# Performance work log

Hardware: AMD Instinct MI355X
Metric: run time of the kernel (lower is better)

Reference implementation:

```python
import jax, jax.numpy as jnp
import numpy as np

# Module configuration (from init_kwargs)
NLAT_IN, NLON_IN = 181, 360
NLAT_OUT, NLON_OUT = 361, 720
KSIZE = 3            # kernel_size of piecewise-linear basis with kernel_shape=3
CIN, COUT = 16, 16   # groups=1 -> groupsize = CIN
NNZ = 8192           # nonzeros in the precomputed psi tensor
B = 1


def setup_inputs() -> dict:
    key = jax.random.key(0)
    ks = jax.random.split(key, 6)
    x = jax.random.normal(ks[0], (B, CIN, NLAT_IN, NLON_IN), dtype=jnp.float32)
    # weight init: sqrt(1/groupsize) * basis init factors * randn
    scale = np.float32(np.sqrt(1.0 / CIN))
    weight = scale * jax.random.normal(ks[1], (COUT, CIN, KSIZE), dtype=jnp.float32)
    bias = jnp.zeros((COUT,), dtype=jnp.float32)
    # synthetic COO psi tensor (geometry-free but structurally identical)
    ker_idx = jax.random.randint(ks[2], (NNZ,), 0, KSIZE, dtype=jnp.int32)
    row_idx = jax.random.randint(ks[3], (NNZ,), 0, NLAT_IN, dtype=jnp.int32)
    col_idx = jax.random.randint(ks[4], (NNZ,), 0, NLAT_OUT * NLON_OUT, dtype=jnp.int32)
    vals = jax.random.uniform(ks[5], (NNZ,), dtype=jnp.float32) * (100.0 / NNZ)
    return {"x": x, "weight": weight, "bias": bias,
            "ker_idx": ker_idx, "row_idx": row_idx, "col_idx": col_idx, "vals": vals}


def reference(x, weight, bias, ker_idx, row_idx, col_idx, vals):
    """DISCO transpose conv on S2: channel-mix einsum, then sparse
    gather-multiply-scatter (adjoint of the longitude-shift-equivariant
    sparse contraction). col_idx encodes (out_lat, lon_offset)."""
    Bb, Cin, H, W = x.shape            # (B, C_in, nlat_in, nlon_in)
    Cout, gs, K = weight.shape
    pscale = NLON_OUT // W             # exact p-shift upsampling factor

    # 1) channel mixing with per-kernel-basis weights (groups=1)
    xw = jnp.einsum('bcxy,ock->bokxy', x, weight)   # [B, Cout, K, nlat_in, nlon_in]

    # 2) gather rows referenced by the sparse psi tensor and scale by vals
    g = xw[:, :, ker_idx, row_idx, :] * vals[None, None, :, None]  # [B, Cout, NNZ, W]

    # 3) scatter-add: each nonzero (k, tin, (tout, p)) contributes the whole
    #    longitude ring of input lat tin to output lat tout at lons (p + po*pscale)
    hi = col_idx // NLON_OUT                      # output latitude  [NNZ]
    p = col_idx % NLON_OUT                        # longitude offset [NNZ]
    lon = (p[:, None] + jnp.arange(W, dtype=p.dtype)[None, :] * pscale) % NLON_OUT  # [NNZ, W]
    flat = (hi[:, None] * NLON_OUT + lon).reshape(-1)  # [NNZ*W]

    out = jnp.zeros((Bb, Cout, NLAT_OUT * NLON_OUT), dtype=x.dtype)
    out = out.at[:, :, flat].add(g.reshape(Bb, Cout, -1))
    out = out.reshape(Bb, Cout, NLAT_OUT, NLON_OUT)
    return out + bias[None, :, None, None]
```

## Files before the change

kernel.cpp:

```cpp
#include <hip/hip_runtime.h>

#define H_IN   181
#define W_IN   360
#define NLAT   361
#define NLON   720
#define CIN    16
#define COUT   16
#define KSZ    3
#define NNZ    8192
#define MAXB   64
#define SLICE_E (KSZ * H_IN * W_IN * 4)
#define NMIX_BLK ((KSZ * H_IN * W_IN + 255) / 256)

static __device__ __forceinline__ unsigned short f2bf(float f) {
    unsigned int u = __float_as_uint(f);
    u = (u + 0x7fffu + ((u >> 16) & 1u)) >> 16;
    return (unsigned short)u;
}
static __device__ __forceinline__ void bf2_to_f2(unsigned int d, float& lo, float& hi) {
    lo = __uint_as_float(d << 16);
    hi = __uint_as_float(d & 0xffff0000u);
}

__global__ __launch_bounds__(256) void mix_bucket_kernel(
    const float* __restrict__ x,
    const float* __restrict__ w,
    const int*   __restrict__ ker_idx,
    const int*   __restrict__ row_idx,
    const int*   __restrict__ col_idx,
    const float* __restrict__ vals,
    unsigned short* __restrict__ xw,
    int*   __restrict__ gcnt,
    int*   __restrict__ gbase,
    int*   __restrict__ gp,
    float* __restrict__ gv)
{
    const int tid = threadIdx.x;

    if (blockIdx.x >= NMIX_BLK) {
        const int ho = blockIdx.x - NMIX_BLK;
        __shared__ int s_cnt;
        if (tid == 0) s_cnt = 0;
        __syncthreads();
        const int4* col4 = (const int4*)col_idx;
        for (int n4 = tid; n4 < NNZ / 4; n4 += 256) {
            const int4 c4 = col4[n4];
#pragma unroll
            for (int j = 0; j < 4; ++j) {
                const int c  = (j == 0) ? c4.x : (j == 1) ? c4.y : (j == 2) ? c4.z : c4.w;
                const int hi = c / NLON;
                if (hi == ho) {
                    const int n    = 4 * n4 + j;
                    const int slot = atomicAdd(&s_cnt, 1);
                    if (slot < MAXB) {
                        gbase[ho * MAXB + slot] = (ker_idx[n] * H_IN + row_idx[n]) * (W_IN * 4);
                        gp[ho * MAXB + slot]    = c - hi * NLON;
                        gv[ho * MAXB + slot]    = vals[n];
                    }
                }
            }
        }
        __syncthreads();
        if (tid == 0) gcnt[ho] = (s_cnt < MAXB) ? s_cnt : MAXB;
        return;
    }

    __shared__ float sw[COUT * CIN * KSZ];
    for (int i = tid; i < COUT * CIN * KSZ; i += 256) sw[i] = w[i];
    __syncthreads();

    const int idx = blockIdx.x * 256 + tid;
    if (idx >= KSZ * H_IN * W_IN) return;
    const int k  = idx / (H_IN * W_IN);
    const int hy = idx - k * (H_IN * W_IN);

    float acc[COUT];
#pragma unroll
    for (int co = 0; co < COUT; ++co) acc[co] = 0.f;

    for (int c = 0; c < CIN; ++c) {
        const float xv = x[c * (H_IN * W_IN) + hy];
#pragma unroll
        for (int co = 0; co < COUT; ++co)
            acc[co] += xv * sw[(co * CIN + c) * KSZ + k];
    }

#pragma unroll
    for (int q = 0; q < 4; ++q) {
        ushort4 b;
        b.x = f2bf(acc[4*q+0]); b.y = f2bf(acc[4*q+1]);
        b.z = f2bf(acc[4*q+2]); b.w = f2bf(acc[4*q+3]);
        *(ushort4*)(xw + (size_t)q * SLICE_E + (size_t)idx * 4) = b;
    }
}

__device__ __forceinline__ void fma4(float4& a, float v, const float4& f) {
    a.x += v * f.x; a.y += v * f.y; a.z += v * f.z; a.w += v * f.w;
}
static __device__ __forceinline__ float4 ld_bf4(const unsigned short* p) {
    const uint2 d = *(const uint2*)p;
    float4 f;
    bf2_to_f2(d.x, f.x, f.y);
    bf2_to_f2(d.y, f.z, f.w);
    return f;
}

__global__ __launch_bounds__(384) void gather_kernel(
    const unsigned short* __restrict__ xw,
    const float* __restrict__ bias,
    const int*   __restrict__ gcnt,
    const int*   __restrict__ gbase,
    const int*   __restrict__ gp,
    const float* __restrict__ gv,
    float* __restrict__ out)
{
    const int ho  = blockIdx.x >> 2;
    const int q   = blockIdx.x & 3;
    const int tid = threadIdx.x;

    __shared__ int   s_base[MAXB];
    __shared__ int   s_p[MAXB];
    __shared__ float s_v[MAXB];

    const int cnt = gcnt[ho];
    if (tid < cnt) {
        s_base[tid] = gbase[ho * MAXB + tid];
        s_p[tid]    = gp[ho * MAXB + tid];
        s_v[tid]    = gv[ho * MAXB + tid];
    }
    __syncthreads();

    if (tid >= 360) return;
    const int lo0 = 2 * tid;

    const float4 bq = ((const float4*)bias)[q];
    float4 accE = bq, accO = bq;
    const unsigned short* slice = xw + (size_t)q * SLICE_E;

    auto entry_y = [&](int p, int b) -> int {
        int d = (lo0 + b) - p;
        if (d < 0) d += NLON;
        return d >> 1;
    };

    int e = 0;
    for (; e + 2 <= cnt; e += 2) {
        const int   p0 = s_p[e],   p1 = s_p[e + 1];
        const float v0 = s_v[e],   v1 = s_v[e + 1];
        const int   b0 = p0 & 1,   b1 = p1 & 1;
        const int   y0 = entry_y(p0, b0);
        const int   y1 = entry_y(p1, b1);
        const float4 f0 = ld_bf4(slice + s_base[e]     + y0 * 4);
        const float4 f1 = ld_bf4(slice + s_base[e + 1] + y1 * 4);
        if (b0 == 0) fma4(accE, v0, f0); else fma4(accO, v0, f0);
        if (b1 == 0) fma4(accE, v1, f1); else fma4(accO, v1, f1);
    }
    if (e < cnt) {
        const int   p = s_p[e];
        const float v = s_v[e];
        const int   b = p & 1;
        const int   y = entry_y(p, b);
        const float4 f = ld_bf4(slice + s_base[e] + y * 4);
        if (b == 0) fma4(accE, v, f); else fma4(accO, v, f);
    }

    const float2 r[4] = { make_float2(accE.x, accO.x), make_float2(accE.y, accO.y),
                          make_float2(accE.z, accO.z), make_float2(accE.w, accO.w) };
#pragma unroll
    for (int j = 0; j < 4; ++j) {
        const int co = 4 * q + j;
        *(float2*)(out + ((size_t)co * NLAT + ho) * NLON + lo0) = r[j];
    }
}

extern "C" void kernel_launch(void* const* d_in, const int* in_sizes, int n_in,
                              void* d_out, int out_size, void* d_ws, size_t ws_size,
                              hipStream_t stream) {
    const float* x       = (const float*)d_in[0];
    const float* weight  = (const float*)d_in[1];
    const float* bias    = (const float*)d_in[2];
    const int*   ker_idx = (const int*)d_in[3];
    const int*   row_idx = (const int*)d_in[4];
    const int*   col_idx = (const int*)d_in[5];
    const float* vals    = (const float*)d_in[6];
    float* out = (float*)d_out;

    unsigned short* xw = (unsigned short*)d_ws;
    int*   gcnt  = (int*)((char*)d_ws + 6255360 + 64);
    int*   gbase = gcnt + 512;
    int*   gp    = gbase + NLAT * MAXB;
    float* gv    = (float*)(gp + NLAT * MAXB);

    mix_bucket_kernel<<<NMIX_BLK + NLAT, 256, 0, stream>>>(
        x, weight, ker_idx, row_idx, col_idx, vals, xw, gcnt, gbase, gp, gv);
    gather_kernel<<<NLAT * 4, 384, 0, stream>>>(xw, bias, gcnt, gbase, gp, gv, out);
}
```

Measured before the change: 99.23 us.

## Fuse mixing and gather into one kernel, applying channel mix after sparse gather

```diff
diff --git a/kernel.cpp b/kernel.cpp
--- a/kernel.cpp
+++ b/kernel.cpp
@@ -9,167 +9,93 @@
 #define KSZ    3
 #define NNZ    8192
 #define MAXB   64
-#define SLICE_E (KSZ * H_IN * W_IN * 4)
-#define NMIX_BLK ((KSZ * H_IN * W_IN + 255) / 256)
+#define XPLANE (H_IN * W_IN)
 
-static __device__ __forceinline__ unsigned short f2bf(float f) {
-    unsigned int u = __float_as_uint(f);
-    u = (u + 0x7fffu + ((u >> 16) & 1u)) >> 16;
-    return (unsigned short)u;
-}
-static __device__ __forceinline__ void bf2_to_f2(unsigned int d, float& lo, float& hi) {
-    lo = __uint_as_float(d << 16);
-    hi = __uint_as_float(d & 0xffff0000u);
-}
-
-__global__ __launch_bounds__(256) void mix_bucket_kernel(
+__global__ __launch_bounds__(384) void fused_disco_kernel(
     const float* __restrict__ x,
     const float* __restrict__ w,
+    const float* __restrict__ bias,
     const int*   __restrict__ ker_idx,
     const int*   __restrict__ row_idx,
     const int*   __restrict__ col_idx,
     const float* __restrict__ vals,
-    unsigned short* __restrict__ xw,
-    int*   __restrict__ gcnt,
-    int*   __restrict__ gbase,
-    int*   __restrict__ gp,
-    float* __restrict__ gv)
+    float* __restrict__ out)
 {
+    const int ho  = blockIdx.x >> 1;
+    const int pe  = blockIdx.x & 1;
     const int tid = threadIdx.x;
 
-    if (blockIdx.x >= NMIX_BLK) {
-        const int ho = blockIdx.x - NMIX_BLK;
-        __shared__ int s_cnt;
-        if (tid == 0) s_cnt = 0;
-        __syncthreads();
-        const int4* col4 = (const int4*)col_idx;
-        for (int n4 = tid; n4 < NNZ / 4; n4 += 256) {
-            const int4 c4 = col4[n4];
-#pragma unroll
-            for (int j = 0; j < 4; ++j) {
-                const int c  = (j == 0) ? c4.x : (j == 1) ? c4.y : (j == 2) ? c4.z : c4.w;
-                const int hi = c / NLON;
-                if (hi == ho) {
-                    const int n    = 4 * n4 + j;
-                    const int slot = atomicAdd(&s_cnt, 1);
-                    if (slot < MAXB) {
-                        gbase[ho * MAXB + slot] = (ker_idx[n] * H_IN + row_idx[n]) * (W_IN * 4);
-                        gp[ho * MAXB + slot]    = c - hi * NLON;
-                        gv[ho * MAXB + slot]    = vals[n];
-                    }
-                }
+    __shared__ int   s_cnt;
+    __shared__ int   s_xrow[MAXB];
+    __shared__ int   s_pk[MAXB];
+    __shared__ float s_v[MAXB];
+
+    if (tid == 0) s_cnt = 0;
+    __syncthreads();
+
+    for (int n = tid; n < NNZ; n += 384) {
+        const int c  = col_idx[n];
+        const int hi = c / NLON;
+        const int p  = c - hi * NLON;
+        if (hi == ho && (p & 1) == pe) {
+            const int slot = atomicAdd(&s_cnt, 1);
+            if (slot < MAXB) {
+                s_xrow[slot] = row_idx[n] * W_IN;
+                s_pk[slot]   = p | (ker_idx[n] << 12);
+                s_v[slot]    = vals[n];
             }
         }
-        __syncthreads();
-        if (tid == 0) gcnt[ho] = (s_cnt < MAXB) ? s_cnt : MAXB;
-        return;
     }
+    __syncthreads();
+    const int cnt = (s_cnt < MAXB) ? s_cnt : MAXB;
 
-    __shared__ float sw[COUT * CIN * KSZ];
-    for (int i = tid; i < COUT * CIN * KSZ; i += 256) sw[i] = w[i];
-    __syncthreads();
+    if (tid >= 360) return;
+    const int lon = 2 * tid + pe;
 
-    const int idx = blockIdx.x * 256 + tid;
-    if (idx >= KSZ * H_IN * W_IN) return;
-    const int k  = idx / (H_IN * W_IN);
-    const int hy = idx - k * (H_IN * W_IN);
+    float g0[CIN], g1[CIN], g2[CIN];
+#pragma unroll
+    for (int c = 0; c < CIN; ++c) { g0[c] = 0.f; g1[c] = 0.f; g2[c] = 0.f; }
 
-    float acc[COUT];
+    for (int e = 0; e < cnt; ++e) {
+        const int   pk = __builtin_amdgcn_readfirstlane(s_pk[e]);
+        const int   xr = __builtin_amdgcn_readfirstlane(s_xrow[e]);
+        const float v  = __uint_as_float(
+                           __builtin_amdgcn_readfirstlane(__float_as_uint(s_v[e])));
+        const int p = pk & 0xfff;
+        const int k = pk >> 12;
+
+        int d = lon - p;
+        if (d < 0) d += NLON;
+        const int y = d >> 1;
+
+        const float* xp = x + xr + y;
+        float xv[CIN];
 #pragma unroll
-    for (int co = 0; co < COUT; ++co) acc[co] = 0.f;
+        for (int c = 0; c < CIN; ++c) xv[c] = xp[c * XPLANE];
 
-    for (int c = 0; c < CIN; ++c) {
-        const float xv = x[c * (H_IN * W_IN) + hy];
+        if (k == 0) {
 #pragma unroll
-        for (int co = 0; co < COUT; ++co)
-            acc[co] += xv * sw[(co * CIN + c) * KSZ + k];
+            for (int c = 0; c < CIN; ++c) g0[c] += v * xv[c];
+        } else if (k == 1) {
+#pragma unroll
+            for (int c = 0; c < CIN; ++c) g1[c] += v * xv[c];
+        } else {
+#pragma unroll
+            for (int c = 0; c < CIN; ++c) g2[c] += v * xv[c];
+        }
     }
 
 #pragma unroll
-    for (int q = 0; q < 4; ++q) {
-        ushort4 b;
-        b.x = f2bf(acc[4*q+0]); b.y = f2bf(acc[4*q+1]);
-        b.z = f2bf(acc[4*q+2]); b.w = f2bf(acc[4*q+3]);
-        *(ushort4*)(xw + (size_t)q * SLICE_E + (size_t)idx * 4) = b;
-    }
-}
-
-__device__ __forceinline__ void fma4(float4& a, float v, const float4& f) {
-    a.x += v * f.x; a.y += v * f.y; a.z += v * f.z; a.w += v * f.w;
-}
-static __device__ __forceinline__ float4 ld_bf4(const unsigned short* p) {
-    const uint2 d = *(const uint2*)p;
-    float4 f;
-    bf2_to_f2(d.x, f.x, f.y);
-    bf2_to_f2(d.y, f.z, f.w);
-    return f;
-}
-
-__global__ __launch_bounds__(384) void gather_kernel(
-    const unsigned short* __restrict__ xw,
-    const float* __restrict__ bias,
-    const int*   __restrict__ gcnt,
-    const int*   __restrict__ gbase,
-    const int*   __restrict__ gp,
-    const float* __restrict__ gv,
-    float* __restrict__ out)
-{
-    const int ho  = blockIdx.x >> 2;
-    const int q   = blockIdx.x & 3;
-    const int tid = threadIdx.x;
-
-    __shared__ int   s_base[MAXB];
-    __shared__ int   s_p[MAXB];
-    __shared__ float s_v[MAXB];
-
-    const int cnt = gcnt[ho];
-    if (tid < cnt) {
-        s_base[tid] = gbase[ho * MAXB + tid];
-        s_p[tid]    = gp[ho * MAXB + tid];
-        s_v[tid]    = gv[ho * MAXB + tid];
-    }
-    __syncthreads();
-
-    if (tid >= 360) return;
-    const int lo0 = 2 * tid;
-
-    const float4 bq = ((const float4*)bias)[q];
-    float4 accE = bq, accO = bq;
-    const unsigned short* slice = xw + (size_t)q * SLICE_E;
-
-    auto entry_y = [&](int p, int b) -> int {
-        int d = (lo0 + b) - p;
-        if (d < 0) d += NLON;
-        return d >> 1;
-    };
-
-    int e = 0;
-    for (; e + 2 <= cnt; e += 2) {
-        const int   p0 = s_p[e],   p1 = s_p[e + 1];
-        const float v0 = s_v[e],   v1 = s_v[e + 1];
-        const int   b0 = p0 & 1,   b1 = p1 & 1;
-        const int   y0 = entry_y(p0, b0);
-        const int   y1 = entry_y(p1, b1);
-        const float4 f0 = ld_bf4(slice + s_base[e]     + y0 * 4);
-        const float4 f1 = ld_bf4(slice + s_base[e + 1] + y1 * 4);
-        if (b0 == 0) fma4(accE, v0, f0); else fma4(accO, v0, f0);
-        if (b1 == 0) fma4(accE, v1, f1); else fma4(accO, v1, f1);
-    }
-    if (e < cnt) {
-        const int   p = s_p[e];
-        const float v = s_v[e];
-        const int   b = p & 1;
-        const int   y = entry_y(p, b);
-        const float4 f = ld_bf4(slice + s_base[e] + y * 4);
-        if (b == 0) fma4(accE, v, f); else fma4(accO, v, f);
-    }
-
-    const float2 r[4] = { make_float2(accE.x, accO.x), make_float2(accE.y, accO.y),
-                          make_float2(accE.z, accO.z), make_float2(accE.w, accO.w) };
+    for (int co = 0; co < COUT; ++co) {
+        float s = bias[co];
 #pragma unroll
-    for (int j = 0; j < 4; ++j) {
-        const int co = 4 * q + j;
-        *(float2*)(out + ((size_t)co * NLAT + ho) * NLON + lo0) = r[j];
+        for (int c = 0; c < CIN; ++c) {
+            const int wb = (co * CIN + c) * KSZ;
+            s += g0[c] * w[wb + 0];
+            s += g1[c] * w[wb + 1];
+            s += g2[c] * w[wb + 2];
+        }
+        out[((size_t)co * NLAT + ho) * NLON + lon] = s;
     }
 }
 
@@ -185,13 +111,8 @@
     const float* vals    = (const float*)d_in[6];
     float* out = (float*)d_out;
 
-    unsigned short* xw = (unsigned short*)d_ws;
-    int*   gcnt  = (int*)((char*)d_ws + 6255360 + 64);
-    int*   gbase = gcnt + 512;
-    int*   gp    = gbase + NLAT * MAXB;
-    float* gv    = (float*)(gp + NLAT * MAXB);
+    (void)d_ws; (void)ws_size;
 
-    mix_bucket_kernel<<<NMIX_BLK + NLAT, 256, 0, stream>>>(
-        x, weight, ker_idx, row_idx, col_idx, vals, xw, gcnt, gbase, gp, gv);
-    gather_kernel<<<NLAT * 4, 384, 0, stream>>>(xw, bias, gcnt, gbase, gp, gv, out);
+    fused_disco_kernel<<<NLAT * 2, 384, 0, stream>>>(
+        x, weight, bias, ker_idx, row_idx, col_idx, vals, out);
 }
```

Measured after the change: 115.7 us. 1.17x slower.

## Split sparse buckets by longitude parity and make gather loop wave-uniform

Applied to the files above, without the earlier changes.

```diff
diff --git a/kernel.cpp b/kernel.cpp
--- a/kernel.cpp
+++ b/kernel.cpp
@@ -8,9 +8,10 @@
 #define COUT   16
 #define KSZ    3
 #define NNZ    8192
-#define MAXB   64
+#define MAXB   48
 #define SLICE_E (KSZ * H_IN * W_IN * 4)
 #define NMIX_BLK ((KSZ * H_IN * W_IN + 255) / 256)
+
 
 static __device__ __forceinline__ unsigned short f2bf(float f) {
     unsigned int u = __float_as_uint(f);
@@ -20,6 +21,22 @@
 static __device__ __forceinline__ void bf2_to_f2(unsigned int d, float& lo, float& hi) {
     lo = __uint_as_float(d << 16);
     hi = __uint_as_float(d & 0xffff0000u);
+}
+static __device__ __forceinline__ int rfl_i(int i) {
+    return __builtin_amdgcn_readfirstlane(i);
+}
+static __device__ __forceinline__ float rfl_f(float f) {
+    return __uint_as_float(__builtin_amdgcn_readfirstlane(__float_as_uint(f)));
+}
+__device__ __forceinline__ void fma4(float4& a, float v, const float4& f) {
+    a.x += v * f.x; a.y += v * f.y; a.z += v * f.z; a.w += v * f.w;
+}
+static __device__ __forceinline__ float4 ld_bf4(const unsigned short* p) {
+    const uint2 d = *(const uint2*)p;
+    float4 f;
+    bf2_to_f2(d.x, f.x, f.y);
+    bf2_to_f2(d.y, f.z, f.w);
+    return f;
 }
 
 __global__ __launch_bounds__(256) void mix_bucket_kernel(
@@ -32,36 +49,53 @@
     unsigned short* __restrict__ xw,
     int*   __restrict__ gcnt,
     int*   __restrict__ gbase,
-    int*   __restrict__ gp,
+    int*   __restrict__ gps,
     float* __restrict__ gv)
 {
     const int tid = threadIdx.x;
 
     if (blockIdx.x >= NMIX_BLK) {
         const int ho = blockIdx.x - NMIX_BLK;
-        __shared__ int s_cnt;
-        if (tid == 0) s_cnt = 0;
+        __shared__ int   s_cnt[2];
+        __shared__ int   s_b [2 * MAXB];
+        __shared__ int   s_ps[2 * MAXB];
+        __shared__ float s_v [2 * MAXB];
+
+        if (tid < 2) s_cnt[tid] = 0;
+        if (tid < 2 * MAXB) { s_b[tid] = 0; s_ps[tid] = 0; s_v[tid] = 0.f; }
         __syncthreads();
-        const int4* col4 = (const int4*)col_idx;
+
+        const int cbase = ho * NLON;
+        const int4* __restrict__ col4 = (const int4*)col_idx;
         for (int n4 = tid; n4 < NNZ / 4; n4 += 256) {
             const int4 c4 = col4[n4];
 #pragma unroll
             for (int j = 0; j < 4; ++j) {
-                const int c  = (j == 0) ? c4.x : (j == 1) ? c4.y : (j == 2) ? c4.z : c4.w;
-                const int hi = c / NLON;
-                if (hi == ho) {
+                const int c = (j == 0) ? c4.x : (j == 1) ? c4.y : (j == 2) ? c4.z : c4.w;
+                const unsigned d = (unsigned)(c - cbase);
+                if (d < (unsigned)NLON) {
                     const int n    = 4 * n4 + j;
-                    const int slot = atomicAdd(&s_cnt, 1);
+                    const int pe   = (int)(d & 1u);
+                    const int slot = atomicAdd(&s_cnt[pe], 1);
                     if (slot < MAXB) {
-                        gbase[ho * MAXB + slot] = (ker_idx[n] * H_IN + row_idx[n]) * (W_IN * 4);
-                        gp[ho * MAXB + slot]    = c - hi * NLON;
-                        gv[ho * MAXB + slot]    = vals[n];
+                        s_b [pe * MAXB + slot] = (ker_idx[n] * H_IN + row_idx[n]) * (W_IN * 4);
+                        s_ps[pe * MAXB + slot] = (int)(d >> 1);
+                        s_v [pe * MAXB + slot] = vals[n];
                     }
                 }
             }
         }
         __syncthreads();
-        if (tid == 0) gcnt[ho] = (s_cnt < MAXB) ? s_cnt : MAXB;
+        if (tid < 2) {
+            int c = s_cnt[tid] < MAXB ? s_cnt[tid] : MAXB;
+            gcnt[ho * 2 + tid] = (c + 3) & ~3;
+        }
+        __syncthreads();
+        for (int i = tid; i < 2 * MAXB; i += 256) {
+            gbase[ho * 2 * MAXB + i] = s_b[i];
+            gps  [ho * 2 * MAXB + i] = s_ps[i];
+            gv   [ho * 2 * MAXB + i] = s_v[i];
+        }
         return;
     }
 
@@ -94,82 +128,77 @@
     }
 }
 
-__device__ __forceinline__ void fma4(float4& a, float v, const float4& f) {
-    a.x += v * f.x; a.y += v * f.y; a.z += v * f.z; a.w += v * f.w;
-}
-static __device__ __forceinline__ float4 ld_bf4(const unsigned short* p) {
-    const uint2 d = *(const uint2*)p;
-    float4 f;
-    bf2_to_f2(d.x, f.x, f.y);
-    bf2_to_f2(d.y, f.z, f.w);
-    return f;
-}
-
 __global__ __launch_bounds__(384) void gather_kernel(
     const unsigned short* __restrict__ xw,
     const float* __restrict__ bias,
     const int*   __restrict__ gcnt,
     const int*   __restrict__ gbase,
-    const int*   __restrict__ gp,
+    const int*   __restrict__ gps,
     const float* __restrict__ gv,
     float* __restrict__ out)
 {
-    const int ho  = blockIdx.x >> 2;
-    const int q   = blockIdx.x & 3;
+    const int bid   = blockIdx.x;
+    const int r     = bid & 7;
+    const int inner = bid >> 3;
+    const int q     = r >> 1;
+    const int ho    = inner * 2 + (r & 1);
+    if (ho >= NLAT) return;
     const int tid = threadIdx.x;
 
-    __shared__ int   s_base[MAXB];
-    __shared__ int   s_p[MAXB];
-    __shared__ float s_v[MAXB];
-
-    const int cnt = gcnt[ho];
-    if (tid < cnt) {
-        s_base[tid] = gbase[ho * MAXB + tid];
-        s_p[tid]    = gp[ho * MAXB + tid];
-        s_v[tid]    = gv[ho * MAXB + tid];
+    __shared__ int   s_c[2];
+    __shared__ int   s_b [2 * MAXB];
+    __shared__ int   s_ps[2 * MAXB];
+    __shared__ float s_v [2 * MAXB];
+
+    if (tid < 2) s_c[tid] = gcnt[ho * 2 + tid];
+    if (tid < 2 * MAXB) {
+        s_b [tid] = gbase[ho * 2 * MAXB + tid];
+        s_ps[tid] = gps  [ho * 2 * MAXB + tid];
+        s_v [tid] = gv   [ho * 2 * MAXB + tid];
     }
     __syncthreads();
 
+    const int cntE = rfl_i(s_c[0]);
+    const int cntO = rfl_i(s_c[1]);
+
     if (tid >= 360) return;
-    const int lo0 = 2 * tid;
+    const int t = tid;
 
     const float4 bq = ((const float4*)bias)[q];
     float4 accE = bq, accO = bq;
-    const unsigned short* slice = xw + (size_t)q * SLICE_E;
-
-    auto entry_y = [&](int p, int b) -> int {
-        int d = (lo0 + b) - p;
-        if (d < 0) d += NLON;
-        return d >> 1;
-    };
-
-    int e = 0;
-    for (; e + 2 <= cnt; e += 2) {
-        const int   p0 = s_p[e],   p1 = s_p[e + 1];
-        const float v0 = s_v[e],   v1 = s_v[e + 1];
-        const int   b0 = p0 & 1,   b1 = p1 & 1;
-        const int   y0 = entry_y(p0, b0);
-        const int   y1 = entry_y(p1, b1);
-        const float4 f0 = ld_bf4(slice + s_base[e]     + y0 * 4);
-        const float4 f1 = ld_bf4(slice + s_base[e + 1] + y1 * 4);
-        if (b0 == 0) fma4(accE, v0, f0); else fma4(accO, v0, f0);
-        if (b1 == 0) fma4(accE, v1, f1); else fma4(accO, v1, f1);
-    }
-    if (e < cnt) {
-        const int   p = s_p[e];
-        const float v = s_v[e];
-        const int   b = p & 1;
-        const int   y = entry_y(p, b);
-        const float4 f = ld_bf4(slice + s_base[e] + y * 4);
-        if (b == 0) fma4(accE, v, f); else fma4(accO, v, f);
-    }
-
-    const float2 r[4] = { make_float2(accE.x, accO.x), make_float2(accE.y, accO.y),
-                          make_float2(accE.z, accO.z), make_float2(accE.w, accO.w) };
+    const unsigned short* __restrict__ slice = xw + (size_t)q * SLICE_E;
+
+#define SEG(PE, CNT, ACC)                                                       \
+    for (int e = 0; e < (CNT); e += 4) {                                        \
+        const int base = (PE) * MAXB + e;                                       \
+        int   b0 = rfl_i(s_b[base+0]), b1 = rfl_i(s_b[base+1]);                 \
+        int   b2 = rfl_i(s_b[base+2]), b3 = rfl_i(s_b[base+3]);                 \
+        int   p0 = rfl_i(s_ps[base+0]), p1 = rfl_i(s_ps[base+1]);               \
+        int   p2 = rfl_i(s_ps[base+2]), p3 = rfl_i(s_ps[base+3]);               \
+        float v0 = rfl_f(s_v[base+0]), v1 = rfl_f(s_v[base+1]);                 \
+        float v2 = rfl_f(s_v[base+2]), v3 = rfl_f(s_v[base+3]);                 \
+        int y0 = t - p0; y0 += (y0 >> 31) & 360;                                \
+        int y1 = t - p1; y1 += (y1 >> 31) & 360;                                \
+        int y2 = t - p2; y2 += (y2 >> 31) & 360;                                \
+        int y3 = t - p3; y3 += (y3 >> 31) & 360;                                \
+        const float4 f0 = ld_bf4(slice + b0 + 4 * y0);                          \
+        const float4 f1 = ld_bf4(slice + b1 + 4 * y1);                          \
+        const float4 f2 = ld_bf4(slice + b2 + 4 * y2);                          \
+        const float4 f3 = ld_bf4(slice + b3 + 4 * y3);                          \
+        fma4(ACC, v0, f0); fma4(ACC, v1, f1);                                   \
+        fma4(ACC, v2, f2); fma4(ACC, v3, f3);                                   \
+    }
+
+    SEG(0, cntE, accE)
+    SEG(1, cntO, accO)
+#undef SEG
+
+    const float2 rr[4] = { make_float2(accE.x, accO.x), make_float2(accE.y, accO.y),
+                           make_float2(accE.z, accO.z), make_float2(accE.w, accO.w) };
 #pragma unroll
     for (int j = 0; j < 4; ++j) {
         const int co = 4 * q + j;
-        *(float2*)(out + ((size_t)co * NLAT + ho) * NLON + lo0) = r[j];
+        *(float2*)(out + ((size_t)co * NLAT + ho) * NLON + 2 * t) = rr[j];
     }
 }
 
@@ -186,12 +215,12 @@
     float* out = (float*)d_out;
 
     unsigned short* xw = (unsigned short*)d_ws;
-    int*   gcnt  = (int*)((char*)d_ws + 6255360 + 64);
-    int*   gbase = gcnt + 512;
-    int*   gp    = gbase + NLAT * MAXB;
-    float* gv    = (float*)(gp + NLAT * MAXB);
+    int*   gcnt  = (int*)((char*)d_ws + 6255360);
+    int*   gbase = gcnt + 1024;
+    int*   gps   = gbase + NLAT * 2 * MAXB;
+    float* gv    = (float*)(gps + NLAT * 2 * MAXB);
 
     mix_bucket_kernel<<<NMIX_BLK + NLAT, 256, 0, stream>>>(
-        x, weight, ker_idx, row_idx, col_idx, vals, xw, gcnt, gbase, gp, gv);
-    gather_kernel<<<NLAT * 4, 384, 0, stream>>>(xw, bias, gcnt, gbase, gp, gv, out);
-}
+        x, weight, ker_idx, row_idx, col_idx, vals, xw, gcnt, gbase, gps, gv);
+    gather_kernel<<<1448, 384, 0, stream>>>(xw, bias, gcnt, gbase, gps, gv, out);
+}
```

After: 93.62 us. -5.7%, faster.
